# Kernel tuning notes

Hardware: AMD Instinct MI355X
Metric: run time of the kernel (lower is better)

Reference implementation:

```python
import jax, jax.numpy as jnp
import numpy as np

D = 1024        # d_hidden
DE = 512        # d_expert (routed)
E = 8           # n_routed_experts
TOP_K = 2
DS = DE * 2     # shared expert width = d_expert * n_shared_experts


def setup_inputs() -> dict:
    key = jax.random.key(0)
    ks = jax.random.split(key, 8)
    s = 1.0 / np.sqrt(D)
    return {
        "x": jax.random.normal(ks[0], (2, 1024, D), dtype=jnp.float32),
        "W_g": jax.random.normal(ks[1], (D, E), dtype=jnp.float32) * s,
        "Wg_e": jax.random.normal(ks[2], (E, D, DE), dtype=jnp.float32) * s,
        "Wu_e": jax.random.normal(ks[3], (E, D, DE), dtype=jnp.float32) * s,
        "Wd_e": jax.random.normal(ks[4], (E, DE, D), dtype=jnp.float32) * (1.0 / np.sqrt(DE)),
        "Wg_s": jax.random.normal(ks[5], (D, DS), dtype=jnp.float32) * s,
        "Wu_s": jax.random.normal(ks[6], (D, DS), dtype=jnp.float32) * s,
        "Wd_s": jax.random.normal(ks[7], (DS, D), dtype=jnp.float32) * (1.0 / np.sqrt(DS)),
    }


def _moe(x, W_g, Wg_e, Wu_e, Wd_e, Wg_s, Wu_s, Wd_s):
    B, T, Dm = x.shape
    N = B * T
    xf = x.reshape(N, Dm)

    # shared expert (SwiGLU)
    shared = (jax.nn.silu(xf @ Wg_s) * (xf @ Wu_s)) @ Wd_s  # [N, D]

    # gating: softmax then top-k (set membership identical to torch sorted=False)
    probs = jax.nn.softmax(xf @ W_g, axis=-1)               # [N, E]
    topk_vals, topk_ids = jax.lax.top_k(probs, TOP_K)       # [N, K]

    # combine weights c[n, e] = sum of topk_vals where routed to expert e
    # (equivalent to the original gather -> weighted scatter_add combine)
    c = jnp.zeros((N, E), dtype=x.dtype)
    c = c.at[jnp.arange(N)[:, None], topk_ids].add(topk_vals)

    # dense per-expert SwiGLU, weighted-combined (same math as gather/scatter loop)
    gate = jax.nn.silu(jnp.einsum('nd,edh->neh', xf, Wg_e))
    up = jnp.einsum('nd,edh->neh', xf, Wu_e)
    routed = jnp.einsum('neh,ne,ehd->nd', gate * up, c, Wd_e)  # [N, D]

    return (shared + routed).reshape(B, T, Dm)


def reference(x, W_g, Wg_e, Wu_e, Wd_e, Wg_s, Wu_s, Wd_s):
    return _moe(x, W_g, Wg_e, Wu_e, Wd_e, Wg_s, Wu_s, Wd_s)
```

## Files before the change

kernel.cpp:

```cpp
#include <hip/hip_runtime.h>
#include <hip/hip_bf16.h>

#define NTOK 2048
#define DIM  1024
#define DEXP 512
#define NEXP 8
#define DSH  1024
#define KH   5120

typedef __hip_bfloat16 bf16;
typedef __attribute__((ext_vector_type(8))) short bf16x8;
typedef __attribute__((ext_vector_type(4))) float floatx4;

__device__ __forceinline__ void gl_lds16(const bf16* g, bf16* l) {
    __builtin_amdgcn_global_load_lds(
        (const __attribute__((address_space(1))) void*)g,
        (__attribute__((address_space(3))) void*)l, 16, 0, 0);
}

__global__ __launch_bounds__(256) void cast_x_kernel(const float* __restrict__ src,
                                                     bf16* __restrict__ dst, int n4) {
    int i = blockIdx.x * 256 + threadIdx.x;
    if (i >= n4) return;
    float4 v = ((const float4*)src)[i];
    struct B4 { bf16 a, b, c, d; };
    B4 o{__float2bfloat16(v.x), __float2bfloat16(v.y),
         __float2bfloat16(v.z), __float2bfloat16(v.w)};
    ((B4*)dst)[i] = o;
}

__global__ __launch_bounds__(256) void pack_weights(
        const float* __restrict__ Wg_s, const float* __restrict__ Wu_s,
        const float* __restrict__ Wg_e, const float* __restrict__ Wu_e,
        const float* __restrict__ Wd_s, const float* __restrict__ Wd_e,
        bf16* __restrict__ Bg, bf16* __restrict__ Bu, bf16* __restrict__ Bd) {
    __shared__ float t[32][33];
    int b = blockIdx.x;
    const float* src; bf16* dst; int C; long dstStride, dstBase; int tilesX;
    if (b < 1024)       { src = Wg_s; dst = Bg; C = 1024; dstStride = 1024; dstBase = 0; tilesX = 32; }
    else if (b < 2048)  { b -= 1024; src = Wu_s; dst = Bu; C = 1024; dstStride = 1024; dstBase = 0; tilesX = 32; }
    else if (b < 6144)  { b -= 2048; int z = b >> 9; b &= 511;
                          src = Wg_e + (long)z * DIM * DEXP; dst = Bg; C = 512;
                          dstStride = 1024; dstBase = (long)(DSH + z * DEXP) * 1024; tilesX = 16; }
    else if (b < 10240) { b -= 6144; int z = b >> 9; b &= 511;
                          src = Wu_e + (long)z * DIM * DEXP; dst = Bu; C = 512;
                          dstStride = 1024; dstBase = (long)(DSH + z * DEXP) * 1024; tilesX = 16; }
    else if (b < 11264) { b -= 10240; src = Wd_s; dst = Bd; C = 1024; dstStride = KH; dstBase = 0; tilesX = 32; }
    else                { b -= 11264; int z = b >> 9; b &= 511;
                          src = Wd_e + (long)z * DEXP * DIM; dst = Bd; C = 1024;
                          dstStride = KH; dstBase = DSH + (long)z * DEXP; tilesX = 32; }
    int tileX = b & (tilesX - 1), tileY = b / tilesX;
    int c0 = tileX * 32, r0 = tileY * 32;
    int tx = threadIdx.x & 31, ty = threadIdx.x >> 5;
#pragma unroll
    for (int i = 0; i < 4; i++)
        t[ty + i * 8][tx] = src[(long)(r0 + ty + i * 8) * C + c0 + tx];
    __syncthreads();
#pragma unroll
    for (int i = 0; i < 4; i++)
        dst[dstBase + (long)(c0 + ty + i * 8) * dstStride + r0 + tx] =
            __float2bfloat16(t[tx][ty + i * 8]);
}

__global__ __launch_bounds__(256) void gate_kernel(const float* __restrict__ x,
                                                   const float* __restrict__ Wg,
                                                   float* __restrict__ c) {
    int t = blockIdx.x * 4 + (threadIdx.x >> 6);
    int lane = threadIdx.x & 63;
    float acc[NEXP] = {0.f, 0.f, 0.f, 0.f, 0.f, 0.f, 0.f, 0.f};
    const float* xr = x + (long)t * DIM;
    for (int d = lane; d < DIM; d += 64) {
        float xv = xr[d];
        float4 w0 = *(const float4*)(Wg + d * NEXP);
        float4 w1 = *(const float4*)(Wg + d * NEXP + 4);
        acc[0] += xv * w0.x; acc[1] += xv * w0.y; acc[2] += xv * w0.z; acc[3] += xv * w0.w;
        acc[4] += xv * w1.x; acc[5] += xv * w1.y; acc[6] += xv * w1.z; acc[7] += xv * w1.w;
    }
#pragma unroll
    for (int e = 0; e < NEXP; e++)
#pragma unroll
        for (int off = 32; off; off >>= 1)
            acc[e] += __shfl_xor(acc[e], off);
    if (lane == 0) {
        float m = acc[0];
#pragma unroll
        for (int e = 1; e < NEXP; e++) m = fmaxf(m, acc[e]);
        float p[NEXP], s = 0.f;
#pragma unroll
        for (int e = 0; e < NEXP; e++) { p[e] = expf(acc[e] - m); s += p[e]; }
        float inv = 1.f / s;
#pragma unroll
        for (int e = 0; e < NEXP; e++) p[e] *= inv;
        int i1 = 0;
#pragma unroll
        for (int e = 1; e < NEXP; e++) if (p[e] > p[i1]) i1 = e;
        int i2 = (i1 == 0) ? 1 : 0;
#pragma unroll
        for (int e = 0; e < NEXP; e++) if (e != i1 && p[e] > p[i2]) i2 = e;
        float* cr = c + (long)t * NEXP;
#pragma unroll
        for (int e = 0; e < NEXP; e++)
            cr[e] = (e == i1) ? p[i1] : ((e == i2) ? p[i2] : 0.f);
    }
}

__global__ __launch_bounds__(256) void gemm_gu(const bf16* __restrict__ X,
                                               const bf16* __restrict__ Bg,
                                               const bf16* __restrict__ Bu,
                                               const float* __restrict__ cbuf,
                                               bf16* __restrict__ H) {
    __shared__ __align__(16) bf16 sA[128 * 32];
    __shared__ __align__(16) bf16 sBg[64 * 32];
    __shared__ __align__(16) bf16 sBu[64 * 32];

    const int bcol0 = blockIdx.x * 64;
    const int row0 = blockIdx.y * 128;
    const int tid = threadIdx.x;
    const int wave = tid >> 6, lane = tid & 63;
    const int wr = wave >> 1, wc = wave & 1;
    const int q = lane >> 4, l15 = lane & 15;
    const int ch0 = wave * 64 + lane;
    const int chA_r = ch0 >> 2, chA_c = ch0 & 3;
    const int ch1 = 256 + ch0;

    floatx4 accG[4][2], accU[4][2];
    const floatx4 z4 = {0.f, 0.f, 0.f, 0.f};
#pragma unroll
    for (int i = 0; i < 4; i++)
#pragma unroll
        for (int j = 0; j < 2; j++) { accG[i][j] = z4; accU[i][j] = z4; }

    for (int k0 = 0; k0 < DIM; k0 += 32) {
        gl_lds16(X + (long)(row0 + chA_r) * DIM + k0 + chA_c * 8,
                 sA + (long)(wave * 64) * 8);
        gl_lds16(X + (long)(row0 + (ch1 >> 2)) * DIM + k0 + (ch1 & 3) * 8,
                 sA + (long)(256 + wave * 64) * 8);
        gl_lds16(Bg + (long)(bcol0 + chA_r) * DIM + k0 + chA_c * 8,
                 sBg + (long)(wave * 64) * 8);
        gl_lds16(Bu + (long)(bcol0 + chA_r) * DIM + k0 + chA_c * 8,
                 sBu + (long)(wave * 64) * 8);
        __syncthreads();

        bf16x8 af[4], bg[2], bu[2];
#pragma unroll
        for (int rt = 0; rt < 4; rt++)
            af[rt] = *(const bf16x8*)(sA + (wr * 64 + rt * 16 + l15) * 32 + q * 8);
#pragma unroll
        for (int ct = 0; ct < 2; ct++) {
            int cb = (wc * 32 + ct * 16 + l15) * 32 + q * 8;
            bg[ct] = *(const bf16x8*)(sBg + cb);
            bu[ct] = *(const bf16x8*)(sBu + cb);
        }
#pragma unroll
        for (int rt = 0; rt < 4; rt++)
#pragma unroll
            for (int ct = 0; ct < 2; ct++) {
                accG[rt][ct] = __builtin_amdgcn_mfma_f32_16x16x32_bf16(af[rt], bg[ct], accG[rt][ct], 0, 0, 0);
                accU[rt][ct] = __builtin_amdgcn_mfma_f32_16x16x32_bf16(af[rt], bu[ct], accU[rt][ct], 0, 0, 0);
            }
        __syncthreads();
    }

    const int isExpert = (bcol0 >= DSH);
    const int e = isExpert ? ((bcol0 - DSH) >> 9) : 0;
    float cv[4][4];
#pragma unroll
    for (int rt = 0; rt < 4; rt++)
#pragma unroll
        for (int r = 0; r < 4; r++) {
            int n = row0 + wr * 64 + rt * 16 + q * 4 + r;
            cv[rt][r] = isExpert ? cbuf[(long)n * NEXP + e] : 1.0f;
        }
#pragma unroll
    for (int rt = 0; rt < 4; rt++)
#pragma unroll
        for (int ct = 0; ct < 2; ct++)
#pragma unroll
            for (int r = 0; r < 4; r++) {
                int n = row0 + wr * 64 + rt * 16 + q * 4 + r;
                int mc = bcol0 + wc * 32 + ct * 16 + l15;
                float g = accG[rt][ct][r];
                float u = accU[rt][ct][r];
                float h = (g / (1.f + __expf(-g))) * u * cv[rt][r];
                H[(long)n * KH + mc] = __float2bfloat16(h);
            }
}

__global__ __launch_bounds__(256) void gemm_down(const bf16* __restrict__ A,
                                                 const bf16* __restrict__ BT,
                                                 float* __restrict__ out) {
    __shared__ __align__(16) bf16 sA[128 * 32];
    __shared__ __align__(16) bf16 sB[128 * 32];
    const int col0 = blockIdx.x * 128;
    const int row0 = blockIdx.y * 128;
    const int kbase = blockIdx.z * (KH / 4);
    const int tid = threadIdx.x;
    const int wave = tid >> 6, lane = tid & 63;
    const int wr = wave >> 1, wc = wave & 1;
    const int q = lane >> 4, l15 = lane & 15;
    const int ch0 = wave * 64 + lane;
    const int ch1 = 256 + ch0;
    const int r0c = ch0 >> 2, c0c = ch0 & 3;
    const int r1c = ch1 >> 2, c1c = ch1 & 3;

    floatx4 acc[4][4];
    const floatx4 z4 = {0.f, 0.f, 0.f, 0.f};
#pragma unroll
    for (int i = 0; i < 4; i++)
#pragma unroll
        for (int j = 0; j < 4; j++) acc[i][j] = z4;

    for (int k0 = kbase; k0 < kbase + KH / 4; k0 += 32) {
        gl_lds16(A + (long)(row0 + r0c) * KH + k0 + c0c * 8, sA + (long)(wave * 64) * 8);
        gl_lds16(A + (long)(row0 + r1c) * KH + k0 + c1c * 8, sA + (long)(256 + wave * 64) * 8);
        gl_lds16(BT + (long)(col0 + r0c) * KH + k0 + c0c * 8, sB + (long)(wave * 64) * 8);
        gl_lds16(BT + (long)(col0 + r1c) * KH + k0 + c1c * 8, sB + (long)(256 + wave * 64) * 8);
        __syncthreads();

        bf16x8 af[4], bb[4];
#pragma unroll
        for (int rt = 0; rt < 4; rt++)
            af[rt] = *(const bf16x8*)(sA + (wr * 64 + rt * 16 + l15) * 32 + q * 8);
#pragma unroll
        for (int ct = 0; ct < 4; ct++)
            bb[ct] = *(const bf16x8*)(sB + (wc * 64 + ct * 16 + l15) * 32 + q * 8);
#pragma unroll
        for (int rt = 0; rt < 4; rt++)
#pragma unroll
            for (int ct = 0; ct < 4; ct++)
                acc[rt][ct] = __builtin_amdgcn_mfma_f32_16x16x32_bf16(af[rt], bb[ct], acc[rt][ct], 0, 0, 0);
        __syncthreads();
    }

#pragma unroll
    for (int rt = 0; rt < 4; rt++)
#pragma unroll
        for (int ct = 0; ct < 4; ct++)
#pragma unroll
            for (int r = 0; r < 4; r++) {
                int n = row0 + wr * 64 + rt * 16 + q * 4 + r;
                int mc = col0 + wc * 64 + ct * 16 + l15;
                atomicAdd(out + (long)n * DIM + mc, acc[rt][ct][r]);
            }
}

extern "C" void kernel_launch(void* const* d_in, const int* in_sizes, int n_in,
                              void* d_out, int out_size, void* d_ws, size_t ws_size,
                              hipStream_t stream) {
    const float* x    = (const float*)d_in[0];
    const float* W_g  = (const float*)d_in[1];
    const float* Wg_e = (const float*)d_in[2];
    const float* Wu_e = (const float*)d_in[3];
    const float* Wd_e = (const float*)d_in[4];
    const float* Wg_s = (const float*)d_in[5];
    const float* Wu_s = (const float*)d_in[6];
    const float* Wd_s = (const float*)d_in[7];
    float* out = (float*)d_out;

    bf16* Xb   = (bf16*)d_ws;
    bf16* Bg   = Xb + (size_t)NTOK * DIM;
    bf16* Bu   = Bg + (size_t)KH * DIM;
    bf16* Bd   = Bu + (size_t)KH * DIM;
    bf16* Hbuf = Bd + (size_t)DIM * KH;
    float* Cbuf = (float*)(Hbuf + (size_t)NTOK * KH);

    hipMemsetAsync(out, 0, (size_t)NTOK * DIM * sizeof(float), stream);
    cast_x_kernel<<<(NTOK * DIM / 4 + 255) / 256, 256, 0, stream>>>(x, Xb, NTOK * DIM / 4);
    pack_weights<<<15360, 256, 0, stream>>>(Wg_s, Wu_s, Wg_e, Wu_e, Wd_s, Wd_e, Bg, Bu, Bd);
    gate_kernel<<<NTOK / 4, 256, 0, stream>>>(x, W_g, Cbuf);
    gemm_gu<<<dim3(KH / 64, NTOK / 128), 256, 0, stream>>>(Xb, Bg, Bu, Cbuf, Hbuf);
    gemm_down<<<dim3(DIM / 128, NTOK / 128, 4), 256, 0, stream>>>(Hbuf, Bd, out);
}
```

Before: 241.9 us.

## Route tokens to experts with sparse token lists instead of dense expert compute

The gate kernel now builds per-expert token lists with atomic counters and combine weights. The gate-up and down GEMMs gather only the routed tokens for each expert and skip empty 128-row tiles, instead of running every token through all 8 experts. An XOR swizzle is also added to the LDS layout to reduce bank conflicts. This removes roughly three quarters of the routed-expert FLOPs. In exchange it adds an indirect row gather, scattered atomic output writes, and a workspace layout that is nondeterministic across runs. Padded tail rows read zero-initialized token indices (token 0) with weight 0, so they add nothing to the output.

```diff
diff --git a/kernel.cpp b/kernel.cpp
--- a/kernel.cpp
+++ b/kernel.cpp
@@ -64,7 +64,9 @@
 
 __global__ __launch_bounds__(256) void gate_kernel(const float* __restrict__ x,
                                                    const float* __restrict__ Wg,
-                                                   float* __restrict__ c) {
+                                                   int* __restrict__ counts,
+                                                   int* __restrict__ tok_list,
+                                                   float* __restrict__ cw) {
     int t = blockIdx.x * 4 + (threadIdx.x >> 6);
     int lane = threadIdx.x & 63;
     float acc[NEXP] = {0.f, 0.f, 0.f, 0.f, 0.f, 0.f, 0.f, 0.f};
@@ -97,31 +99,58 @@
         int i2 = (i1 == 0) ? 1 : 0;
 #pragma unroll
         for (int e = 0; e < NEXP; e++) if (e != i1 && p[e] > p[i2]) i2 = e;
-        float* cr = c + (long)t * NEXP;
-#pragma unroll
-        for (int e = 0; e < NEXP; e++)
-            cr[e] = (e == i1) ? p[i1] : ((e == i2) ? p[i2] : 0.f);
-    }
-}
-
-__global__ __launch_bounds__(256) void gemm_gu(const bf16* __restrict__ X,
-                                               const bf16* __restrict__ Bg,
-                                               const bf16* __restrict__ Bu,
-                                               const float* __restrict__ cbuf,
-                                               bf16* __restrict__ H) {
+        int s1 = atomicAdd(counts + i1, 1);
+        tok_list[i1 * NTOK + s1] = t;
+        cw[i1 * NTOK + s1] = p[i1];
+        int s2 = atomicAdd(counts + i2, 1);
+        tok_list[i2 * NTOK + s2] = t;
+        cw[i2 * NTOK + s2] = p[i2];
+    }
+}
+
+__global__ __launch_bounds__(256) void gu_all(const bf16* __restrict__ X,
+                                              const bf16* __restrict__ Bg,
+                                              const bf16* __restrict__ Bu,
+                                              const int* __restrict__ counts,
+                                              const int* __restrict__ tok_list,
+                                              const float* __restrict__ cw,
+                                              bf16* __restrict__ Hs,
+                                              bf16* __restrict__ He) {
     __shared__ __align__(16) bf16 sA[128 * 32];
     __shared__ __align__(16) bf16 sBg[64 * 32];
     __shared__ __align__(16) bf16 sBu[64 * 32];
 
-    const int bcol0 = blockIdx.x * 64;
-    const int row0 = blockIdx.y * 128;
+    const int b = blockIdx.x;
+    const bool routed = b < 1024;
+    int e = 0, m, c;
+    if (routed) {
+        e = b >> 7; m = (b >> 3) & 15; c = b & 7;
+        if (m * 128 >= counts[e]) return;
+    } else {
+        int bs = b - 1024; m = bs >> 4; c = bs & 15;
+    }
+    const int colB0 = routed ? (DSH + e * DEXP + c * 64) : c * 64;
+
     const int tid = threadIdx.x;
     const int wave = tid >> 6, lane = tid & 63;
     const int wr = wave >> 1, wc = wave & 1;
     const int q = lane >> 4, l15 = lane & 15;
-    const int ch0 = wave * 64 + lane;
-    const int chA_r = ch0 >> 2, chA_c = ch0 & 3;
-    const int ch1 = 256 + ch0;
+    const int xorv = (l15 >> 1) & 3;
+    const int koff = (q ^ xorv) * 8;
+
+    const int r0 = tid >> 2, c4 = tid & 3;
+    const int r1 = r0 + 64;
+    const int c4s = c4 ^ ((r0 >> 1) & 3);
+    long aRow0, aRow1;
+    if (routed) {
+        const int* tl = tok_list + e * NTOK + m * 128;
+        aRow0 = (long)tl[r0] * DIM;
+        aRow1 = (long)tl[r1] * DIM;
+    } else {
+        aRow0 = (long)(m * 128 + r0) * DIM;
+        aRow1 = (long)(m * 128 + r1) * DIM;
+    }
+    const long bRow = (long)(colB0 + r0) * DIM;
 
     floatx4 accG[4][2], accU[4][2];
     const floatx4 z4 = {0.f, 0.f, 0.f, 0.f};
@@ -131,23 +160,19 @@
         for (int j = 0; j < 2; j++) { accG[i][j] = z4; accU[i][j] = z4; }
 
     for (int k0 = 0; k0 < DIM; k0 += 32) {
-        gl_lds16(X + (long)(row0 + chA_r) * DIM + k0 + chA_c * 8,
-                 sA + (long)(wave * 64) * 8);
-        gl_lds16(X + (long)(row0 + (ch1 >> 2)) * DIM + k0 + (ch1 & 3) * 8,
-                 sA + (long)(256 + wave * 64) * 8);
-        gl_lds16(Bg + (long)(bcol0 + chA_r) * DIM + k0 + chA_c * 8,
-                 sBg + (long)(wave * 64) * 8);
-        gl_lds16(Bu + (long)(bcol0 + chA_r) * DIM + k0 + chA_c * 8,
-                 sBu + (long)(wave * 64) * 8);
+        gl_lds16(X + aRow0 + k0 + c4s * 8, sA + (wave * 64) * 8);
+        gl_lds16(X + aRow1 + k0 + c4s * 8, sA + (256 + wave * 64) * 8);
+        gl_lds16(Bg + bRow + k0 + c4s * 8, sBg + (wave * 64) * 8);
+        gl_lds16(Bu + bRow + k0 + c4s * 8, sBu + (wave * 64) * 8);
         __syncthreads();
 
         bf16x8 af[4], bg[2], bu[2];
 #pragma unroll
         for (int rt = 0; rt < 4; rt++)
-            af[rt] = *(const bf16x8*)(sA + (wr * 64 + rt * 16 + l15) * 32 + q * 8);
+            af[rt] = *(const bf16x8*)(sA + (wr * 64 + rt * 16 + l15) * 32 + koff);
 #pragma unroll
         for (int ct = 0; ct < 2; ct++) {
-            int cb = (wc * 32 + ct * 16 + l15) * 32 + q * 8;
+            int cb = (wc * 32 + ct * 16 + l15) * 32 + koff;
             bg[ct] = *(const bf16x8*)(sBg + cb);
             bu[ct] = *(const bf16x8*)(sBu + cb);
         }
@@ -161,15 +186,13 @@
         __syncthreads();
     }
 
-    const int isExpert = (bcol0 >= DSH);
-    const int e = isExpert ? ((bcol0 - DSH) >> 9) : 0;
-    float cv[4][4];
+    float wv[4][4];
 #pragma unroll
     for (int rt = 0; rt < 4; rt++)
 #pragma unroll
         for (int r = 0; r < 4; r++) {
-            int n = row0 + wr * 64 + rt * 16 + q * 4 + r;
-            cv[rt][r] = isExpert ? cbuf[(long)n * NEXP + e] : 1.0f;
+            int srow = wr * 64 + rt * 16 + q * 4 + r;
+            wv[rt][r] = routed ? cw[e * NTOK + m * 128 + srow] : 1.0f;
         }
 #pragma unroll
     for (int rt = 0; rt < 4; rt++)
@@ -177,70 +200,100 @@
         for (int ct = 0; ct < 2; ct++)
 #pragma unroll
             for (int r = 0; r < 4; r++) {
-                int n = row0 + wr * 64 + rt * 16 + q * 4 + r;
-                int mc = bcol0 + wc * 32 + ct * 16 + l15;
+                int srow = wr * 64 + rt * 16 + q * 4 + r;
+                int colLoc = c * 64 + wc * 32 + ct * 16 + l15;
                 float g = accG[rt][ct][r];
                 float u = accU[rt][ct][r];
-                float h = (g / (1.f + __expf(-g))) * u * cv[rt][r];
-                H[(long)n * KH + mc] = __float2bfloat16(h);
+                float h = (g / (1.f + __expf(-g))) * u * wv[rt][r];
+                if (routed)
+                    He[((long)e * NTOK + m * 128 + srow) * DEXP + colLoc] = __float2bfloat16(h);
+                else
+                    Hs[(long)(m * 128 + srow) * DSH + colLoc] = __float2bfloat16(h);
             }
 }
 
-__global__ __launch_bounds__(256) void gemm_down(const bf16* __restrict__ A,
-                                                 const bf16* __restrict__ BT,
-                                                 float* __restrict__ out) {
+__global__ __launch_bounds__(256) void down_all(const bf16* __restrict__ Hs,
+                                                const bf16* __restrict__ He,
+                                                const bf16* __restrict__ Bd,
+                                                const int* __restrict__ counts,
+                                                const int* __restrict__ tok_list,
+                                                float* __restrict__ out) {
     __shared__ __align__(16) bf16 sA[128 * 32];
-    __shared__ __align__(16) bf16 sB[128 * 32];
-    const int col0 = blockIdx.x * 128;
-    const int row0 = blockIdx.y * 128;
-    const int kbase = blockIdx.z * (KH / 4);
+    __shared__ __align__(16) bf16 sB[64 * 32];
+
+    const int b = blockIdx.x;
+    const bool routed = b < 2048;
+    int e = 0, m, cc;
+    if (routed) {
+        e = b >> 8; m = (b >> 4) & 15; cc = b & 15;
+        if (m * 128 >= counts[e]) return;
+    } else {
+        int bs = b - 2048; m = bs >> 4; cc = bs & 15;
+    }
+    const bf16* A = routed ? He + (long)e * NTOK * DEXP : Hs;
+    const int astr = routed ? DEXP : DSH;
+    const int ksteps = routed ? (DEXP / 32) : (DSH / 32);
+    const int kg0 = routed ? (DSH + e * DEXP) : 0;
+
     const int tid = threadIdx.x;
     const int wave = tid >> 6, lane = tid & 63;
     const int wr = wave >> 1, wc = wave & 1;
     const int q = lane >> 4, l15 = lane & 15;
-    const int ch0 = wave * 64 + lane;
-    const int ch1 = 256 + ch0;
-    const int r0c = ch0 >> 2, c0c = ch0 & 3;
-    const int r1c = ch1 >> 2, c1c = ch1 & 3;
-
-    floatx4 acc[4][4];
+    const int xorv = (l15 >> 1) & 3;
+    const int koff = (q ^ xorv) * 8;
+
+    const int r0 = tid >> 2, c4 = tid & 3;
+    const int r1 = r0 + 64;
+    const int c4s = c4 ^ ((r0 >> 1) & 3);
+    const long aRow0 = (long)(m * 128 + r0) * astr;
+    const long aRow1 = (long)(m * 128 + r1) * astr;
+    const long bRow = (long)(cc * 64 + r0) * KH + kg0;
+
+    floatx4 acc[4][2];
     const floatx4 z4 = {0.f, 0.f, 0.f, 0.f};
 #pragma unroll
     for (int i = 0; i < 4; i++)
 #pragma unroll
-        for (int j = 0; j < 4; j++) acc[i][j] = z4;
-
-    for (int k0 = kbase; k0 < kbase + KH / 4; k0 += 32) {
-        gl_lds16(A + (long)(row0 + r0c) * KH + k0 + c0c * 8, sA + (long)(wave * 64) * 8);
-        gl_lds16(A + (long)(row0 + r1c) * KH + k0 + c1c * 8, sA + (long)(256 + wave * 64) * 8);
-        gl_lds16(BT + (long)(col0 + r0c) * KH + k0 + c0c * 8, sB + (long)(wave * 64) * 8);
-        gl_lds16(BT + (long)(col0 + r1c) * KH + k0 + c1c * 8, sB + (long)(256 + wave * 64) * 8);
+        for (int j = 0; j < 2; j++) acc[i][j] = z4;
+
+    for (int ks = 0; ks < ksteps; ks++) {
+        const int k0 = ks * 32;
+        gl_lds16(A + aRow0 + k0 + c4s * 8, sA + (wave * 64) * 8);
+        gl_lds16(A + aRow1 + k0 + c4s * 8, sA + (256 + wave * 64) * 8);
+        gl_lds16(Bd + bRow + k0 + c4s * 8, sB + (wave * 64) * 8);
         __syncthreads();
 
-        bf16x8 af[4], bb[4];
+        bf16x8 af[4], bb[2];
 #pragma unroll
         for (int rt = 0; rt < 4; rt++)
-            af[rt] = *(const bf16x8*)(sA + (wr * 64 + rt * 16 + l15) * 32 + q * 8);
-#pragma unroll
-        for (int ct = 0; ct < 4; ct++)
-            bb[ct] = *(const bf16x8*)(sB + (wc * 64 + ct * 16 + l15) * 32 + q * 8);
+            af[rt] = *(const bf16x8*)(sA + (wr * 64 + rt * 16 + l15) * 32 + koff);
+#pragma unroll
+        for (int ct = 0; ct < 2; ct++)
+            bb[ct] = *(const bf16x8*)(sB + (wc * 32 + ct * 16 + l15) * 32 + koff);
 #pragma unroll
         for (int rt = 0; rt < 4; rt++)
 #pragma unroll
-            for (int ct = 0; ct < 4; ct++)
+            for (int ct = 0; ct < 2; ct++)
                 acc[rt][ct] = __builtin_amdgcn_mfma_f32_16x16x32_bf16(af[rt], bb[ct], acc[rt][ct], 0, 0, 0);
         __syncthreads();
     }
 
+    int nrow[4][4];
 #pragma unroll
     for (int rt = 0; rt < 4; rt++)
 #pragma unroll
-        for (int ct = 0; ct < 4; ct++)
+        for (int r = 0; r < 4; r++) {
+            int srow = wr * 64 + rt * 16 + q * 4 + r;
+            nrow[rt][r] = routed ? tok_list[e * NTOK + m * 128 + srow] : (m * 128 + srow);
+        }
+#pragma unroll
+    for (int rt = 0; rt < 4; rt++)
+#pragma unroll
+        for (int ct = 0; ct < 2; ct++)
 #pragma unroll
             for (int r = 0; r < 4; r++) {
-                int n = row0 + wr * 64 + rt * 16 + q * 4 + r;
-                int mc = col0 + wc * 64 + ct * 16 + l15;
-                atomicAdd(out + (long)n * DIM + mc, acc[rt][ct][r]);
+                int mc = cc * 64 + wc * 32 + ct * 16 + l15;
+                atomicAdd(out + (long)nrow[rt][r] * DIM + mc, acc[rt][ct][r]);
             }
 }
 
@@ -257,17 +310,23 @@
     const float* Wd_s = (const float*)d_in[7];
     float* out = (float*)d_out;
 
-    bf16* Xb   = (bf16*)d_ws;
-    bf16* Bg   = Xb + (size_t)NTOK * DIM;
-    bf16* Bu   = Bg + (size_t)KH * DIM;
-    bf16* Bd   = Bu + (size_t)KH * DIM;
-    bf16* Hbuf = Bd + (size_t)DIM * KH;
-    float* Cbuf = (float*)(Hbuf + (size_t)NTOK * KH);
+    bf16* Xb = (bf16*)d_ws;
+    bf16* Bg = Xb + (size_t)NTOK * DIM;
+    bf16* Bu = Bg + (size_t)KH * DIM;
+    bf16* Bd = Bu + (size_t)KH * DIM;
+    bf16* Hs = Bd + (size_t)DIM * KH;
+    bf16* He = Hs + (size_t)NTOK * DSH;
+    int*  counts   = (int*)(He + (size_t)NEXP * NTOK * DEXP);
+    int*  tok_list = counts + NEXP;
+    float* cw      = (float*)(tok_list + NEXP * NTOK);
+    const size_t metaBytes = sizeof(int) * NEXP + sizeof(int) * NEXP * NTOK
+                           + sizeof(float) * NEXP * NTOK;
 
     hipMemsetAsync(out, 0, (size_t)NTOK * DIM * sizeof(float), stream);
+    hipMemsetAsync(counts, 0, metaBytes, stream);
     cast_x_kernel<<<(NTOK * DIM / 4 + 255) / 256, 256, 0, stream>>>(x, Xb, NTOK * DIM / 4);
     pack_weights<<<15360, 256, 0, stream>>>(Wg_s, Wu_s, Wg_e, Wu_e, Wd_s, Wd_e, Bg, Bu, Bd);
-    gate_kernel<<<NTOK / 4, 256, 0, stream>>>(x, W_g, Cbuf);
-    gemm_gu<<<dim3(KH / 64, NTOK / 128), 256, 0, stream>>>(Xb, Bg, Bu, Cbuf, Hbuf);
-    gemm_down<<<dim3(DIM / 128, NTOK / 128, 4), 256, 0, stream>>>(Hbuf, Bd, out);
-}
+    gate_kernel<<<NTOK / 4, 256, 0, stream>>>(x, W_g, counts, tok_list, cw);
+    gu_all<<<1280, 256, 0, stream>>>(Xb, Bg, Bu, counts, tok_list, cw, Hs, He);
+    down_all<<<2304, 256, 0, stream>>>(Hs, He, Bd, counts, tok_list, out);
+}
```

Result: slower. 299.7 us (+23.9%).
